# Optimization experiments

Hardware: AMD Instinct MI355X
Metric: run time of the kernel (lower is better)

## Reference

```python
import jax, jax.numpy as jnp
import numpy as np

N_NODES = 100000


def gcn_conv(x, edge_index, W, b):
    """PyG GCNConv: h = x W^T; add self-loops; symmetric deg^-1/2 norm; scatter-add; + bias."""
    n = x.shape[0]
    src = jnp.concatenate([edge_index[0], jnp.arange(n)])  # self-loops appended
    dst = jnp.concatenate([edge_index[1], jnp.arange(n)])
    deg = jax.ops.segment_sum(jnp.ones_like(dst, dtype=x.dtype), dst, num_segments=n)
    dinv = jnp.where(deg > 0, jax.lax.rsqrt(deg), 0.0)
    norm = dinv[src] * dinv[dst]                             # [E+n]
    h = x @ W.T                                              # [n, out]
    msg = norm[:, None] * h[src]                             # [E+n, out] gather
    out = jax.ops.segment_sum(msg, dst, num_segments=n)      # scatter-add
    return out + b


def setup_inputs() -> dict:
    key = jax.random.key(0)
    ks = jax.random.split(key, 10)
    input_dim, gnn_hidden, tree_hidden, num_classes = 128, 64, 32, 8
    n_edges = 3200000
    x = jax.random.normal(ks[0], (N_NODES, input_dim), dtype=jnp.float32)
    edge_index = jax.random.randint(ks[1], (2, n_edges), 0, N_NODES, dtype=jnp.int64)
    # GCNConv params (PyG Linear weight is [out, in], glorot-ish scale)
    W1 = jax.random.normal(ks[2], (gnn_hidden, input_dim), dtype=jnp.float32) / np.sqrt(input_dim)
    b1 = jnp.zeros((gnn_hidden,), dtype=jnp.float32)
    W2 = jax.random.normal(ks[3], (tree_hidden, gnn_hidden), dtype=jnp.float32) / np.sqrt(gnn_hidden)
    b2 = jnp.zeros((tree_hidden,), dtype=jnp.float32)
    # SoftDecisionTree params (torch.randn init in source)
    gate_w = jax.random.normal(ks[4], (tree_hidden, tree_hidden), dtype=jnp.float32)
    gate_b = jnp.zeros((tree_hidden,), dtype=jnp.float32)
    leaf_w = jax.random.normal(ks[5], (tree_hidden, num_classes), dtype=jnp.float32)
    return {"x": x, "edge_index": edge_index, "W1": W1, "b1": b1, "W2": W2,
            "b2": b2, "gate_w": gate_w, "gate_b": gate_b, "leaf_w": leaf_w}


def reference(x, edge_index, W1, b1, W2, b2, gate_w, gate_b, leaf_w):
    h = jax.nn.relu(gcn_conv(x, edge_index, W1, b1))
    h = gcn_conv(h, edge_index, W2, b2)
    gates = jax.nn.sigmoid(h @ gate_w.T + gate_b)
    return gates @ leaf_w
```

## Files before the change

kernel.cpp:

```cpp
#include <hip/hip_runtime.h>
#include <math.h>

#define IN_DIM 128
#define H1 64
#define H2 32
#define NC 8
#define SCAN_CH 1024
#define NB_MAX 512
#define BLK 512
#define CAP 12288

typedef unsigned int u32;

__device__ __forceinline__ float bf_lo(u32 u) { return __uint_as_float(u << 16); }
__device__ __forceinline__ float bf_hi(u32 u) { return __uint_as_float(u & 0xffff0000u); }
__device__ __forceinline__ unsigned short f2b(float f) {
  u32 u = __float_as_uint(f);
  u += 0x7fffu + ((u >> 16) & 1u);
  return (unsigned short)(u >> 16);
}


__global__ __launch_bounds__(256) void k_hist(const int* __restrict__ dst,
                                              int* __restrict__ bh,
                                              int E, int EPB, int NBk) {
  __shared__ int h[NB_MAX];
  int k = blockIdx.x, tid = threadIdx.x;
  for (int i = tid; i < NBk; i += 256) h[i] = 0;
  __syncthreads();
  int st = k * EPB, en = min(E, st + EPB);
  for (int i = st + tid; i < en; i += 256)
    atomicAdd(&h[((u32)dst[i]) >> 8], 1);
  __syncthreads();
  for (int b = tid; b < NBk; b += 256) bh[b * BLK + k] = h[b];
}


__global__ __launch_bounds__(256) void k_gsc1(const int* __restrict__ A,
                                              int* __restrict__ bsum, int L) {
  int b = blockIdx.x, tid = threadIdx.x;
  int i0 = b * SCAN_CH + tid * 4;
  int s = 0;
  if (i0 + 3 < L) {
    int4 v = *(const int4*)(A + i0);
    s = v.x + v.y + v.z + v.w;
  } else {
    for (int i = i0; i < L; ++i) s += A[i];
  }
  __shared__ int red[256];
  red[tid] = s;
  __syncthreads();
  for (int d = 128; d > 0; d >>= 1) {
    if (tid < d) red[tid] += red[tid + d];
    __syncthreads();
  }
  if (tid == 0) bsum[b] = red[0];
}

__global__ __launch_bounds__(256) void k_gsc2(const int* __restrict__ bsum,
                                              int* __restrict__ bbase,
                                              int* __restrict__ S, int nbk, int L) {
  __shared__ int part[256];
  int tid = threadIdx.x;
  int chunk = (nbk + 255) / 256;
  int st = tid * chunk, en = min(st + chunk, nbk);
  int s = 0;
  for (int i = st; i < en; ++i) s += bsum[i];
  part[tid] = s;
  __syncthreads();
  for (int d = 1; d < 256; d <<= 1) {
    int t = (tid >= d) ? part[tid - d] : 0;
    __syncthreads();
    part[tid] += t;
    __syncthreads();
  }
  int base = (tid == 0) ? 0 : part[tid - 1];
  for (int i = st; i < en; ++i) { bbase[i] = base; base += bsum[i]; }
  if (tid == 255) S[L] = part[255];
}

__global__ __launch_bounds__(256) void k_gsc3(const int* __restrict__ A,
                                              const int* __restrict__ bbase,
                                              int* __restrict__ S, int L) {
  int b = blockIdx.x, tid = threadIdx.x;
  int i0 = b * SCAN_CH + tid * 4;
  int e0 = 0, e1 = 0, e2 = 0, e3 = 0;
  if (i0 + 3 < L) {
    int4 v = *(const int4*)(A + i0);
    e0 = v.x; e1 = v.y; e2 = v.z; e3 = v.w;
  } else {
    if (i0 + 0 < L) e0 = A[i0 + 0];
    if (i0 + 1 < L) e1 = A[i0 + 1];
    if (i0 + 2 < L) e2 = A[i0 + 2];
    if (i0 + 3 < L) e3 = A[i0 + 3];
  }
  __shared__ int part[256];
  part[tid] = e0 + e1 + e2 + e3;
  __syncthreads();
  for (int d = 1; d < 256; d <<= 1) {
    int t = (tid >= d) ? part[tid - d] : 0;
    __syncthreads();
    part[tid] += t;
    __syncthreads();
  }
  int base = bbase[b] + ((tid == 0) ? 0 : part[tid - 1]);
  int o0 = base, o1 = o0 + e0, o2 = o1 + e1, o3 = o2 + e2;
  if (i0 + 3 < L) {
    int4 o; o.x = o0; o.y = o1; o.z = o2; o.w = o3;
    *(int4*)(S + i0) = o;
  } else {
    if (i0 + 0 < L) S[i0 + 0] = o0;
    if (i0 + 1 < L) S[i0 + 1] = o1;
    if (i0 + 2 < L) S[i0 + 2] = o2;
    if (i0 + 3 < L) S[i0 + 3] = o3;
  }
}


__global__ __launch_bounds__(256) void k_scatter(const int* __restrict__ src,
                                                 const int* __restrict__ dst,
                                                 const int* __restrict__ S,
                                                 u32* __restrict__ packed,
                                                 int E, int EPB, int NBk) {
  __shared__ int cur[NB_MAX];
  int k = blockIdx.x, tid = threadIdx.x;
  for (int b = tid; b < NBk; b += 256) cur[b] = S[b * BLK + k];
  __syncthreads();
  int st = k * EPB, en = min(E, st + EPB);
  for (int i = st + tid; i < en; i += 256) {
    int d = dst[i];
    int b = ((u32)d) >> 8;
    int pos = atomicAdd(&cur[b], 1);
    packed[pos] = (((u32)d & 255u) << 17) | (u32)src[i];
  }
}


__global__ __launch_bounds__(256) void k_build(const u32* __restrict__ packed,
                                               const int* __restrict__ S,
                                               int* __restrict__ csr,
                                               int* __restrict__ off,
                                               float* __restrict__ dinv,
                                               int n, int NBk) {
  __shared__ int cnt[256];
  __shared__ int tmp[256];
  __shared__ int cur[256];
  __shared__ int sbuf[CAP];
  int b = blockIdx.x, tid = threadIdx.x;
  int r0 = S[b * BLK];
  int r1 = S[(b + 1) * BLK];
  int m = r1 - r0;
  cnt[tid] = 0;
  __syncthreads();
  for (int i = r0 + tid; i < r1; i += 256)
    atomicAdd(&cnt[packed[i] >> 17], 1);
  __syncthreads();
  int v = cnt[tid];
  tmp[tid] = v;
  __syncthreads();
  for (int d = 1; d < 256; d <<= 1) {
    int t = (tid >= d) ? tmp[tid - d] : 0;
    __syncthreads();
    tmp[tid] += t;
    __syncthreads();
  }
  int rel = tmp[tid] - v;
  int node = b * 256 + tid;
  if (node < n) {
    off[node] = r0 + rel;
    dinv[node] = rsqrtf((float)(v + 1));
  }
  if (b == NBk - 1 && tid == 0) off[n] = r1;
  cur[tid] = rel;
  __syncthreads();
  if (m <= CAP) {
    for (int i = r0 + tid; i < r1; i += 256) {
      u32 u = packed[i];
      int pos = atomicAdd(&cur[u >> 17], 1);
      sbuf[pos] = (int)(u & 0x1FFFFu);
    }
    __syncthreads();
    for (int j = tid; j < m; j += 256)
      csr[r0 + j] = sbuf[j];
  } else {
    for (int i = r0 + tid; i < r1; i += 256) {
      u32 u = packed[i];
      int pos = atomicAdd(&cur[u >> 17], 1);
      csr[r0 + pos] = (int)(u & 0x1FFFFu);
    }
  }
}


__global__ void k_proj1(const float4* __restrict__ x4, const float* __restrict__ W1,
                        const float* __restrict__ dinv,
                        unsigned short* __restrict__ h1p, int n) {
  __shared__ float xs[16][IN_DIM];
  __shared__ float wt[IN_DIM][H1 + 1];
  int tid = threadIdx.x;
  int row0 = blockIdx.x * 16;

  for (int i = tid; i < (H1 * IN_DIM / 4); i += 256) {
    float4 w = ((const float4*)W1)[i];
    int o = (i * 4) / IN_DIM;
    int k = (i * 4) % IN_DIM;
    wt[k + 0][o] = w.x; wt[k + 1][o] = w.y; wt[k + 2][o] = w.z; wt[k + 3][o] = w.w;
  }
  for (int i = tid; i < 16 * IN_DIM / 4; i += 256) {
    int r = (i * 4) / IN_DIM, k = (i * 4) % IN_DIM;
    int row = row0 + r;
    if (row < n)
      *((float4*)&xs[r][k]) = x4[(size_t)row * (IN_DIM / 4) + k / 4];
  }
  __syncthreads();

  int o = tid & 63, rq = tid >> 6;
  float a0 = 0.f, a1 = 0.f, a2 = 0.f, a3 = 0.f;
  for (int k = 0; k < IN_DIM; ++k) {
    float w = wt[k][o];
    a0 += xs[rq * 4 + 0][k] * w;
    a1 += xs[rq * 4 + 1][k] * w;
    a2 += xs[rq * 4 + 2][k] * w;
    a3 += xs[rq * 4 + 3][k] * w;
  }
  int r = row0 + rq * 4;
  if (r + 0 < n) h1p[(size_t)(r + 0) * H1 + o] = f2b(a0 * dinv[r + 0]);
  if (r + 1 < n) h1p[(size_t)(r + 1) * H1 + o] = f2b(a1 * dinv[r + 1]);
  if (r + 2 < n) h1p[(size_t)(r + 2) * H1 + o] = f2b(a2 * dinv[r + 2]);
  if (r + 3 < n) h1p[(size_t)(r + 3) * H1 + o] = f2b(a3 * dinv[r + 3]);
}


#define ACC8(v) do { \
    a0 += bf_lo((v).x); a1 += bf_hi((v).x); \
    a2 += bf_lo((v).y); a3 += bf_hi((v).y); \
    a4 += bf_lo((v).z); a5 += bf_hi((v).z); \
    a6 += bf_lo((v).w); a7 += bf_hi((v).w); } while (0)

#define RED8(m) do { \
    a0 += __shfl_xor(a0, m, 64); a1 += __shfl_xor(a1, m, 64); \
    a2 += __shfl_xor(a2, m, 64); a3 += __shfl_xor(a3, m, 64); \
    a4 += __shfl_xor(a4, m, 64); a5 += __shfl_xor(a5, m, 64); \
    a6 += __shfl_xor(a6, m, 64); a7 += __shfl_xor(a7, m, 64); } while (0)

__global__ __launch_bounds__(256) void k_agg64_proj2(
    const u32* __restrict__ hp,
    const float* __restrict__ dinv,
    const int* __restrict__ off, const int* __restrict__ csr,
    const float* __restrict__ b1, const float* __restrict__ W2,
    unsigned short* __restrict__ h2p, int n) {
  __shared__ float wt[H1][H2 + 1];
  __shared__ float rows[4][2][H1];
  __shared__ float b1s[H1];
  int tid = threadIdx.x;

  for (int i = tid; i < H2 * H1 / 4; i += 256) {
    float4 w = ((const float4*)W2)[i];
    int o = (i * 4) / H1, k = (i * 4) % H1;
    wt[k + 0][o] = w.x; wt[k + 1][o] = w.y; wt[k + 2][o] = w.z; wt[k + 3][o] = w.w;
  }
  if (tid < 16) ((float4*)b1s)[tid] = ((const float4*)b1)[tid];
  __syncthreads();

  int lane = tid & 63;
  int wv = __builtin_amdgcn_readfirstlane(tid >> 6);
  int p0n = (blockIdx.x * 4 + wv) * 2;
  int p0c = min(p0n, n - 1);
  int p1c = min(p0n + 1, n - 1);
  int g = lane >> 3, j = lane & 7;
  int nh = g >> 2;

  int tt = 0;
  if (lane < 3) tt = off[min(p0n + lane, n)];
  int r00 = __shfl(tt, 0, 64);
  int r01 = __shfl(tt, 1, 64);
  int r11 = __shfl(tt, 2, 64);
  float dv = 0.f;
  if (lane < 2) dv = dinv[min(p0n + lane, n - 1)];
  float d0 = __shfl(dv, 0, 64), d1 = __shfl(dv, 1, 64);

  const uint4* __restrict__ hp4 = (const uint4*)hp;
  float a0 = 0.f, a1 = 0.f, a2 = 0.f, a3 = 0.f,
        a4 = 0.f, a5 = 0.f, a6 = 0.f, a7 = 0.f;

  if ((g & 3) == 0) {
    uint4 v = hp4[(size_t)(nh ? p1c : p0c) * (H1 / 8) + j];
    ACC8(v);
  }

  int mx = max(r01 - r00, r11 - r01);
  for (int kk = 0; kk * 16 < mx; ++kk) {
    int b0 = r00 + 16 * kk, b1e = r01 + 16 * kk;
    int ci = (lane < 32) ? min(b0 + (lane & 15), r01 - 1)
                         : min(b1e + (lane & 15), r11 - 1);
    int s = csr[max(ci, 0)];
#pragma unroll
    for (int it = 0; it < 4; ++it) {
      int e = it * 4 + (g & 3);
      int sv = __shfl(s, (nh ? 32 : 0) + e, 64);
      int eidx = (nh ? b1e : b0) + e;
      int lim = nh ? r11 : r01;
      if (eidx < lim) {
        uint4 v = hp4[(size_t)sv * (H1 / 8) + j];
        ACC8(v);
      }
    }
  }
  RED8(8); RED8(16);

  float d = (lane < 32) ? d0 : d1;
  if ((lane & 31) < 8) {
    int jj = lane & 7, nn = lane >> 5;
    float4 v0, v1;
    v0.x = fmaxf(a0 * d + b1s[8 * jj + 0], 0.f);
    v0.y = fmaxf(a1 * d + b1s[8 * jj + 1], 0.f);
    v0.z = fmaxf(a2 * d + b1s[8 * jj + 2], 0.f);
    v0.w = fmaxf(a3 * d + b1s[8 * jj + 3], 0.f);
    v1.x = fmaxf(a4 * d + b1s[8 * jj + 4], 0.f);
    v1.y = fmaxf(a5 * d + b1s[8 * jj + 5], 0.f);
    v1.z = fmaxf(a6 * d + b1s[8 * jj + 6], 0.f);
    v1.w = fmaxf(a7 * d + b1s[8 * jj + 7], 0.f);
    *(float4*)&rows[wv][nn][8 * jj + 0] = v0;
    *(float4*)&rows[wv][nn][8 * jj + 4] = v1;
  }
  __syncthreads();

  int node = lane >> 5, o = lane & 31;
  float a = 0.f;
#pragma unroll
  for (int k = 0; k < H1; ++k) a += rows[wv][node][k] * wt[k][o];
  int wout = p0n + node;
  if (wout < n) h2p[(size_t)wout * H2 + o] = f2b(a * ((node) ? d1 : d0));
}


__global__ __launch_bounds__(256) void k_agg32_tree(
    const u32* __restrict__ hp,
    const float* __restrict__ dinv,
    const int* __restrict__ off, const int* __restrict__ csr,
    const float* __restrict__ b2, const float* __restrict__ gate_w,
    const float* __restrict__ gate_b, const float* __restrict__ leaf_w,
    float* __restrict__ out, int n) {
  __shared__ float gwt[H2][H2 + 1];
  __shared__ float lws[H2][NC + 1];
  __shared__ float rowh[4][2][H2];
  __shared__ float rowg[4][2][H2];
  __shared__ float b2s[H2];
  int tid = threadIdx.x;

  {
    float4 w = ((const float4*)gate_w)[tid];
    int jj = (tid * 4) / H2, k = (tid * 4) % H2;
    gwt[k + 0][jj] = w.x; gwt[k + 1][jj] = w.y; gwt[k + 2][jj] = w.z; gwt[k + 3][jj] = w.w;
  }
  lws[tid >> 3][tid & 7] = leaf_w[tid];
  if (tid < 8) ((float4*)b2s)[tid] = ((const float4*)b2)[tid];
  __syncthreads();

  int lane = tid & 63;
  int wv = __builtin_amdgcn_readfirstlane(tid >> 6);
  int p0n = (blockIdx.x * 4 + wv) * 2;
  int p0c = min(p0n, n - 1);
  int p1c = min(p0n + 1, n - 1);
  int g = lane >> 2, j = lane & 3;
  int nh = g >> 3;

  int tt = 0;
  if (lane < 3) tt = off[min(p0n + lane, n)];
  int r00 = __shfl(tt, 0, 64);
  int r01 = __shfl(tt, 1, 64);
  int r11 = __shfl(tt, 2, 64);
  float dv = 0.f;
  if (lane < 2) dv = dinv[min(p0n + lane, n - 1)];
  float d0 = __shfl(dv, 0, 64), d1 = __shfl(dv, 1, 64);

  const uint4* __restrict__ hp4 = (const uint4*)hp;
  float a0 = 0.f, a1 = 0.f, a2 = 0.f, a3 = 0.f,
        a4 = 0.f, a5 = 0.f, a6 = 0.f, a7 = 0.f;

  if ((g & 7) == 0) {
    uint4 v = hp4[(size_t)(nh ? p1c : p0c) * (H2 / 8) + j];
    ACC8(v);
  }

  int mx = max(r01 - r00, r11 - r01);
  for (int kk = 0; kk * 16 < mx; ++kk) {
    int b0 = r00 + 16 * kk, b1e = r01 + 16 * kk;
    int ci = (lane < 32) ? min(b0 + (lane & 15), r01 - 1)
                         : min(b1e + (lane & 15), r11 - 1);
    int s = csr[max(ci, 0)];
#pragma unroll
    for (int it = 0; it < 2; ++it) {
      int e = it * 8 + (g & 7);
      int sv = __shfl(s, (nh ? 32 : 0) + e, 64);
      int eidx = (nh ? b1e : b0) + e;
      int lim = nh ? r11 : r01;
      if (eidx < lim) {
        uint4 v = hp4[(size_t)sv * (H2 / 8) + j];
        ACC8(v);
      }
    }
  }
  RED8(4); RED8(8); RED8(16);

  float d = (lane < 32) ? d0 : d1;
  if ((lane & 31) < 4) {
    int jj = lane & 3, nn = lane >> 5;
    float4 v0, v1;
    v0.x = a0 * d + b2s[8 * jj + 0];
    v0.y = a1 * d + b2s[8 * jj + 1];
    v0.z = a2 * d + b2s[8 * jj + 2];
    v0.w = a3 * d + b2s[8 * jj + 3];
    v1.x = a4 * d + b2s[8 * jj + 4];
    v1.y = a5 * d + b2s[8 * jj + 5];
    v1.z = a6 * d + b2s[8 * jj + 6];
    v1.w = a7 * d + b2s[8 * jj + 7];
    *(float4*)&rowh[wv][nn][8 * jj + 0] = v0;
    *(float4*)&rowh[wv][nn][8 * jj + 4] = v1;
  }
  __syncthreads();

  int node = lane >> 5, f = lane & 31;
  float gacc = 0.f;
#pragma unroll
  for (int k = 0; k < H2; ++k) gacc += rowh[wv][node][k] * gwt[k][f];
  rowg[wv][node][f] = 1.0f / (1.0f + __expf(-(gacc + gate_b[f])));
  __syncthreads();

  int c = lane & 7, gi = (lane >> 3) & 3;
  float a = 0.f;
#pragma unroll
  for (int j8 = 0; j8 < 8; ++j8) {
    int jj = gi * 8 + j8;
    a += rowg[wv][node][jj] * lws[jj][c];
  }
  a += __shfl_xor(a, 8, 64);
  a += __shfl_xor(a, 16, 64);
  int wout = p0n + node;
  if ((lane & 31) < 8 && wout < n) out[(size_t)wout * NC + c] = a;
}


static inline size_t align256(size_t x) { return (x + 255) & ~(size_t)255; }

extern "C" void kernel_launch(void* const* d_in, const int* in_sizes, int n_in,
                              void* d_out, int out_size, void* d_ws, size_t ws_size,
                              hipStream_t stream) {
  const float* x  = (const float*)d_in[0];
  const int*   ei = (const int*)d_in[1];
  const float* W1 = (const float*)d_in[2];
  const float* b1 = (const float*)d_in[3];
  const float* W2 = (const float*)d_in[4];
  const float* b2 = (const float*)d_in[5];
  const float* gw = (const float*)d_in[6];
  const float* gb = (const float*)d_in[7];
  const float* lw = (const float*)d_in[8];
  float* out = (float*)d_out;

  int n = in_sizes[0] / IN_DIM;
  int E = in_sizes[1] / 2;
  const int* src  = ei;
  const int* dstp = ei + E;

  int NBk = (n + 255) >> 8;
  int EPB = (E + BLK - 1) / BLK;
  int L   = NBk * BLK;
  int nbs = (L + SCAN_CH - 1) / SCAN_CH;

  char* w = (char*)d_ws;
  unsigned short* h1p = (unsigned short*)w;  w += align256((size_t)n * H1 * 2);
  unsigned short* h2p = (unsigned short*)w;  w += align256((size_t)n * H2 * 2);
  int* csr    = (int*)w;   w += align256((size_t)E * 4);
  u32* packed = (u32*)w;   w += align256((size_t)E * 4);
  int* bh     = (int*)w;   w += align256(((size_t)L + 1) * 4);
  int* S      = (int*)w;   w += align256(((size_t)L + 1) * 4);
  int* bsum   = (int*)w;   w += align256((size_t)nbs * 4);
  int* bbase  = (int*)w;   w += align256((size_t)nbs * 4);
  float* dinv = (float*)w; w += align256((size_t)n * 4);
  int* off    = (int*)w;   w += align256(((size_t)n + 1) * 4);

  int gw8 = (n + 7) / 8;

  k_hist<<<BLK, 256, 0, stream>>>(dstp, bh, E, EPB, NBk);
  k_gsc1<<<nbs, 256, 0, stream>>>(bh, bsum, L);
  k_gsc2<<<1, 256, 0, stream>>>(bsum, bbase, S, nbs, L);
  k_gsc3<<<nbs, 256, 0, stream>>>(bh, bbase, S, L);
  k_scatter<<<BLK, 256, 0, stream>>>(src, dstp, S, packed, E, EPB, NBk);
  k_build<<<NBk, 256, 0, stream>>>(packed, S, csr, off, dinv, n, NBk);

  k_proj1<<<(n + 15) / 16, 256, 0, stream>>>((const float4*)x, W1, dinv, h1p, n);
  k_agg64_proj2<<<gw8, 256, 0, stream>>>((const u32*)h1p, dinv, off, csr, b1, W2, h2p, n);
  k_agg32_tree<<<gw8, 256, 0, stream>>>((const u32*)h2p, dinv, off, csr, b2, gw, gb, lw, out, n);
}
```

Before: 350.9 us.

## Fuse CSR build stages: single-block scan, global degree, scatter+proj1 merge, sorted neighbors

The histogram kernel now also counts per-node degree with global atomics, which lets dinv be computed early. The three-pass scan collapses into one kernel whose block 0 scans the histogram while the other blocks compute dinv. The edge scatter and the first projection are merged into a single launch with block-range dispatch so they can run concurrently. The build step now sorts each node's neighbors coarsely by source range, which should improve gather locality in the aggregation kernels. The costs are extra global atomics on deg, a single-block scan, larger shared arrays in the build kernel, and the CAP reduction to 10240 that pushes more buckets onto the slower fallback path.

```diff
diff --git a/kernel.cpp b/kernel.cpp
--- a/kernel.cpp
+++ b/kernel.cpp
@@ -5,10 +5,9 @@
 #define H1 64
 #define H2 32
 #define NC 8
-#define SCAN_CH 1024
 #define NB_MAX 512
 #define BLK 512
-#define CAP 12288
+#define CAP 10240
 
 typedef unsigned int u32;
 
@@ -21,185 +20,95 @@
 }
 
 
-__global__ __launch_bounds__(256) void k_hist(const int* __restrict__ dst,
-                                              int* __restrict__ bh,
-                                              int E, int EPB, int NBk) {
+__global__ __launch_bounds__(256) void k_hist2(const int* __restrict__ dst,
+                                               int* __restrict__ bh,
+                                               int* __restrict__ deg,
+                                               int E, int EPB, int NBk) {
   __shared__ int h[NB_MAX];
   int k = blockIdx.x, tid = threadIdx.x;
   for (int i = tid; i < NBk; i += 256) h[i] = 0;
   __syncthreads();
   int st = k * EPB, en = min(E, st + EPB);
-  for (int i = st + tid; i < en; i += 256)
-    atomicAdd(&h[((u32)dst[i]) >> 8], 1);
-  __syncthreads();
-  for (int b = tid; b < NBk; b += 256) bh[b * BLK + k] = h[b];
-}
-
-
-__global__ __launch_bounds__(256) void k_gsc1(const int* __restrict__ A,
-                                              int* __restrict__ bsum, int L) {
-  int b = blockIdx.x, tid = threadIdx.x;
-  int i0 = b * SCAN_CH + tid * 4;
-  int s = 0;
-  if (i0 + 3 < L) {
-    int4 v = *(const int4*)(A + i0);
-    s = v.x + v.y + v.z + v.w;
-  } else {
-    for (int i = i0; i < L; ++i) s += A[i];
-  }
-  __shared__ int red[256];
-  red[tid] = s;
-  __syncthreads();
-  for (int d = 128; d > 0; d >>= 1) {
-    if (tid < d) red[tid] += red[tid + d];
-    __syncthreads();
-  }
-  if (tid == 0) bsum[b] = red[0];
-}
-
-__global__ __launch_bounds__(256) void k_gsc2(const int* __restrict__ bsum,
-                                              int* __restrict__ bbase,
-                                              int* __restrict__ S, int nbk, int L) {
-  __shared__ int part[256];
-  int tid = threadIdx.x;
-  int chunk = (nbk + 255) / 256;
-  int st = tid * chunk, en = min(st + chunk, nbk);
-  int s = 0;
-  for (int i = st; i < en; ++i) s += bsum[i];
-  part[tid] = s;
-  __syncthreads();
-  for (int d = 1; d < 256; d <<= 1) {
-    int t = (tid >= d) ? part[tid - d] : 0;
-    __syncthreads();
-    part[tid] += t;
-    __syncthreads();
-  }
-  int base = (tid == 0) ? 0 : part[tid - 1];
-  for (int i = st; i < en; ++i) { bbase[i] = base; base += bsum[i]; }
-  if (tid == 255) S[L] = part[255];
-}
-
-__global__ __launch_bounds__(256) void k_gsc3(const int* __restrict__ A,
-                                              const int* __restrict__ bbase,
-                                              int* __restrict__ S, int L) {
-  int b = blockIdx.x, tid = threadIdx.x;
-  int i0 = b * SCAN_CH + tid * 4;
-  int e0 = 0, e1 = 0, e2 = 0, e3 = 0;
-  if (i0 + 3 < L) {
-    int4 v = *(const int4*)(A + i0);
-    e0 = v.x; e1 = v.y; e2 = v.z; e3 = v.w;
-  } else {
-    if (i0 + 0 < L) e0 = A[i0 + 0];
-    if (i0 + 1 < L) e1 = A[i0 + 1];
-    if (i0 + 2 < L) e2 = A[i0 + 2];
-    if (i0 + 3 < L) e3 = A[i0 + 3];
-  }
-  __shared__ int part[256];
-  part[tid] = e0 + e1 + e2 + e3;
-  __syncthreads();
-  for (int d = 1; d < 256; d <<= 1) {
-    int t = (tid >= d) ? part[tid - d] : 0;
-    __syncthreads();
-    part[tid] += t;
-    __syncthreads();
-  }
-  int base = bbase[b] + ((tid == 0) ? 0 : part[tid - 1]);
-  int o0 = base, o1 = o0 + e0, o2 = o1 + e1, o3 = o2 + e2;
-  if (i0 + 3 < L) {
-    int4 o; o.x = o0; o.y = o1; o.z = o2; o.w = o3;
-    *(int4*)(S + i0) = o;
-  } else {
-    if (i0 + 0 < L) S[i0 + 0] = o0;
-    if (i0 + 1 < L) S[i0 + 1] = o1;
-    if (i0 + 2 < L) S[i0 + 2] = o2;
-    if (i0 + 3 < L) S[i0 + 3] = o3;
-  }
-}
-
-
-__global__ __launch_bounds__(256) void k_scatter(const int* __restrict__ src,
-                                                 const int* __restrict__ dst,
-                                                 const int* __restrict__ S,
-                                                 u32* __restrict__ packed,
-                                                 int E, int EPB, int NBk) {
-  __shared__ int cur[NB_MAX];
-  int k = blockIdx.x, tid = threadIdx.x;
-  for (int b = tid; b < NBk; b += 256) cur[b] = S[b * BLK + k];
-  __syncthreads();
-  int st = k * EPB, en = min(E, st + EPB);
   for (int i = st + tid; i < en; i += 256) {
     int d = dst[i];
-    int b = ((u32)d) >> 8;
-    int pos = atomicAdd(&cur[b], 1);
-    packed[pos] = (((u32)d & 255u) << 17) | (u32)src[i];
-  }
-}
-
-
-__global__ __launch_bounds__(256) void k_build(const u32* __restrict__ packed,
-                                               const int* __restrict__ S,
-                                               int* __restrict__ csr,
-                                               int* __restrict__ off,
-                                               float* __restrict__ dinv,
-                                               int n, int NBk) {
-  __shared__ int cnt[256];
-  __shared__ int tmp[256];
-  __shared__ int cur[256];
-  __shared__ int sbuf[CAP];
-  int b = blockIdx.x, tid = threadIdx.x;
-  int r0 = S[b * BLK];
-  int r1 = S[(b + 1) * BLK];
-  int m = r1 - r0;
-  cnt[tid] = 0;
-  __syncthreads();
-  for (int i = r0 + tid; i < r1; i += 256)
-    atomicAdd(&cnt[packed[i] >> 17], 1);
-  __syncthreads();
-  int v = cnt[tid];
-  tmp[tid] = v;
-  __syncthreads();
-  for (int d = 1; d < 256; d <<= 1) {
-    int t = (tid >= d) ? tmp[tid - d] : 0;
+    atomicAdd(&h[((u32)d) >> 8], 1);
+    atomicAdd(&deg[d], 1);
+  }
+  __syncthreads();
+  for (int b = tid; b < NBk; b += 256) bh[b * BLK + k] = h[b];
+}
+
+
+__global__ __launch_bounds__(1024) void k_scan_dinv(const int* __restrict__ A,
+                                                    int* __restrict__ S,
+                                                    const int* __restrict__ deg,
+                                                    float* __restrict__ dinv,
+                                                    int L, int n) {
+  if (blockIdx.x == 0) {
+    __shared__ int part[1024];
+    int t = threadIdx.x;
+    int C = (L + 1023) >> 10;
+    C = (C + 3) & ~3;
+    int st = t * C, en = min(st + C, L);
+    int s = 0;
+    int i = st;
+    for (; i + 3 < en; i += 4) {
+      int4 v = *(const int4*)(A + i);
+      s += v.x + v.y + v.z + v.w;
+    }
+    for (; i < en; ++i) s += A[i];
+    part[t] = s;
     __syncthreads();
-    tmp[tid] += t;
-    __syncthreads();
-  }
-  int rel = tmp[tid] - v;
-  int node = b * 256 + tid;
-  if (node < n) {
-    off[node] = r0 + rel;
-    dinv[node] = rsqrtf((float)(v + 1));
-  }
-  if (b == NBk - 1 && tid == 0) off[n] = r1;
-  cur[tid] = rel;
-  __syncthreads();
-  if (m <= CAP) {
-    for (int i = r0 + tid; i < r1; i += 256) {
-      u32 u = packed[i];
-      int pos = atomicAdd(&cur[u >> 17], 1);
-      sbuf[pos] = (int)(u & 0x1FFFFu);
-    }
-    __syncthreads();
-    for (int j = tid; j < m; j += 256)
-      csr[r0 + j] = sbuf[j];
+    for (int d = 1; d < 1024; d <<= 1) {
+      int v = (t >= d) ? part[t - d] : 0;
+      __syncthreads();
+      part[t] += v;
+      __syncthreads();
+    }
+    int base = (t == 0) ? 0 : part[t - 1];
+    i = st;
+    for (; i + 3 < en; i += 4) {
+      int4 v = *(const int4*)(A + i);
+      int4 o;
+      o.x = base; o.y = base + v.x; o.z = o.y + v.y; o.w = o.z + v.z;
+      *(int4*)(S + i) = o;
+      base = o.w + v.w;
+    }
+    for (; i < en; ++i) { S[i] = base; base += A[i]; }
+    if (t == 1023) S[L] = part[1023];
   } else {
-    for (int i = r0 + tid; i < r1; i += 256) {
-      u32 u = packed[i];
-      int pos = atomicAdd(&cur[u >> 17], 1);
-      csr[r0 + pos] = (int)(u & 0x1FFFFu);
-    }
-  }
-}
-
-
-__global__ void k_proj1(const float4* __restrict__ x4, const float* __restrict__ W1,
-                        const float* __restrict__ dinv,
-                        unsigned short* __restrict__ h1p, int n) {
+    int i = (blockIdx.x - 1) * 1024 + threadIdx.x;
+    if (i < n) dinv[i] = rsqrtf((float)(deg[i] + 1));
+  }
+}
+
+
+__global__ __launch_bounds__(256) void k_scat_proj(
+    const int* __restrict__ src, const int* __restrict__ dst,
+    const int* __restrict__ S, u32* __restrict__ packed,
+    int E, int EPB, int NBk,
+    const float4* __restrict__ x4, const float* __restrict__ W1,
+    const float* __restrict__ dinv, unsigned short* __restrict__ h1p, int n) {
+  __shared__ int cur[NB_MAX];
   __shared__ float xs[16][IN_DIM];
   __shared__ float wt[IN_DIM][H1 + 1];
   int tid = threadIdx.x;
-  int row0 = blockIdx.x * 16;
-
+
+  if ((int)blockIdx.x < BLK) {
+    int k = blockIdx.x;
+    for (int b = tid; b < NBk; b += 256) cur[b] = S[b * BLK + k];
+    __syncthreads();
+    int st = k * EPB, en = min(E, st + EPB);
+    for (int i = st + tid; i < en; i += 256) {
+      int d = dst[i];
+      int b = ((u32)d) >> 8;
+      int pos = atomicAdd(&cur[b], 1);
+      packed[pos] = (((u32)d & 255u) << 17) | (u32)src[i];
+    }
+    return;
+  }
+
+  int row0 = ((int)blockIdx.x - BLK) * 16;
   for (int i = tid; i < (H1 * IN_DIM / 4); i += 256) {
     float4 w = ((const float4*)W1)[i];
     int o = (i * 4) / IN_DIM;
@@ -228,6 +137,70 @@
   if (r + 1 < n) h1p[(size_t)(r + 1) * H1 + o] = f2b(a1 * dinv[r + 1]);
   if (r + 2 < n) h1p[(size_t)(r + 2) * H1 + o] = f2b(a2 * dinv[r + 2]);
   if (r + 3 < n) h1p[(size_t)(r + 3) * H1 + o] = f2b(a3 * dinv[r + 3]);
+}
+
+
+__global__ __launch_bounds__(256) void k_build3(const u32* __restrict__ packed,
+                                                const int* __restrict__ S,
+                                                u32* __restrict__ csr2,
+                                                int* __restrict__ off,
+                                                int n, int NBk) {
+  __shared__ int bins[2048];
+  __shared__ int cur[2048];
+  __shared__ int scn[256];
+  __shared__ u32 sbuf[CAP];
+  int b = blockIdx.x, tid = threadIdx.x;
+  int r0 = S[b * BLK];
+  int r1 = S[(b + 1) * BLK];
+  int m = r1 - r0;
+  for (int i = tid; i < 2048; i += 256) bins[i] = 0;
+  __syncthreads();
+  for (int i = r0 + tid; i < r1; i += 256) {
+    u32 p = packed[i];
+    int key = (int)((p >> 17) << 3) | (int)((p & 0x1FFFFu) >> 14);
+    atomicAdd(&bins[key], 1);
+  }
+  __syncthreads();
+  int s = 0;
+#pragma unroll
+  for (int u = 0; u < 8; ++u) s += bins[tid * 8 + u];
+  scn[tid] = s;
+  __syncthreads();
+  for (int d = 1; d < 256; d <<= 1) {
+    int t = (tid >= d) ? scn[tid - d] : 0;
+    __syncthreads();
+    scn[tid] += t;
+    __syncthreads();
+  }
+  int base = scn[tid] - s;
+  int node = b * 256 + tid;
+  if (node < n) off[node] = r0 + base;
+  if (b == NBk - 1 && tid == 0) off[n] = r1;
+#pragma unroll
+  for (int u = 0; u < 8; ++u) {
+    int k = tid * 8 + u;
+    cur[k] = base;
+    base += bins[k];
+  }
+  __syncthreads();
+  if (m <= CAP) {
+    for (int i = r0 + tid; i < r1; i += 256) {
+      u32 p = packed[i];
+      int key = (int)((p >> 17) << 3) | (int)((p & 0x1FFFFu) >> 14);
+      int pos = atomicAdd(&cur[key], 1);
+      sbuf[pos] = p & 0x1FFFFu;
+    }
+    __syncthreads();
+    for (int j = tid; j < m; j += 256)
+      csr2[r0 + j] = sbuf[j];
+  } else {
+    for (int i = r0 + tid; i < r1; i += 256) {
+      u32 p = packed[i];
+      int key = (int)((p >> 17) << 3) | (int)((p & 0x1FFFFu) >> 14);
+      int pos = atomicAdd(&cur[key], 1);
+      csr2[r0 + pos] = p & 0x1FFFFu;
+    }
+  }
 }
 
 
@@ -465,30 +438,29 @@
   int NBk = (n + 255) >> 8;
   int EPB = (E + BLK - 1) / BLK;
   int L   = NBk * BLK;
-  int nbs = (L + SCAN_CH - 1) / SCAN_CH;
 
   char* w = (char*)d_ws;
   unsigned short* h1p = (unsigned short*)w;  w += align256((size_t)n * H1 * 2);
   unsigned short* h2p = (unsigned short*)w;  w += align256((size_t)n * H2 * 2);
-  int* csr    = (int*)w;   w += align256((size_t)E * 4);
+  u32* csr2   = (u32*)w;   w += align256((size_t)E * 4);
   u32* packed = (u32*)w;   w += align256((size_t)E * 4);
   int* bh     = (int*)w;   w += align256(((size_t)L + 1) * 4);
   int* S      = (int*)w;   w += align256(((size_t)L + 1) * 4);
-  int* bsum   = (int*)w;   w += align256((size_t)nbs * 4);
-  int* bbase  = (int*)w;   w += align256((size_t)nbs * 4);
+  int* deg    = (int*)w;   w += align256((size_t)n * 4);
   float* dinv = (float*)w; w += align256((size_t)n * 4);
   int* off    = (int*)w;   w += align256(((size_t)n + 1) * 4);
 
   int gw8 = (n + 7) / 8;
-
-  k_hist<<<BLK, 256, 0, stream>>>(dstp, bh, E, EPB, NBk);
-  k_gsc1<<<nbs, 256, 0, stream>>>(bh, bsum, L);
-  k_gsc2<<<1, 256, 0, stream>>>(bsum, bbase, S, nbs, L);
-  k_gsc3<<<nbs, 256, 0, stream>>>(bh, bbase, S, L);
-  k_scatter<<<BLK, 256, 0, stream>>>(src, dstp, S, packed, E, EPB, NBk);
-  k_build<<<NBk, 256, 0, stream>>>(packed, S, csr, off, dinv, n, NBk);
-
-  k_proj1<<<(n + 15) / 16, 256, 0, stream>>>((const float4*)x, W1, dinv, h1p, n);
-  k_agg64_proj2<<<gw8, 256, 0, stream>>>((const u32*)h1p, dinv, off, csr, b1, W2, h2p, n);
-  k_agg32_tree<<<gw8, 256, 0, stream>>>((const u32*)h2p, dinv, off, csr, b2, gw, gb, lw, out, n);
-}
+  int pblk = (n + 15) / 16;
+
+  hipMemsetAsync(deg, 0, (size_t)n * 4, stream);
+  k_hist2<<<BLK, 256, 0, stream>>>(dstp, bh, deg, E, EPB, NBk);
+  k_scan_dinv<<<1 + (n + 1023) / 1024, 1024, 0, stream>>>(bh, S, deg, dinv, L, n);
+  k_scat_proj<<<BLK + pblk, 256, 0, stream>>>(src, dstp, S, packed, E, EPB, NBk,
+                                              (const float4*)x, W1, dinv, h1p, n);
+  k_build3<<<NBk, 256, 0, stream>>>(packed, S, csr2, off, n, NBk);
+  k_agg64_proj2<<<gw8, 256, 0, stream>>>((const u32*)h1p, dinv, off, (const int*)csr2,
+                                         b1, W2, h2p, n);
+  k_agg32_tree<<<gw8, 256, 0, stream>>>((const u32*)h2p, dinv, off, (const int*)csr2,
+                                        b2, gw, gb, lw, out, n);
+}
```

Measured after the change: 558.0 us. 1.59x slower.

## Sort CSR neighbors by coarse source bucket and vectorize proj1 shared reads

Applied to the files above, without the earlier changes.

The CSR build now bins edges by destination node plus the top bits of the source index (8 sub-buckets per node), so each node's neighbor list is roughly sorted by source region. This is meant to improve gather locality in the two aggregation kernels. The shared staging buffer is shrunk to make room for the larger bin arrays, so more buckets may fall back to direct global scatter. The proj1 inner loop is also changed to read rows of x with float4 from shared memory and unroll four k-steps.

```diff
diff --git a/kernel.cpp b/kernel.cpp
--- a/kernel.cpp
+++ b/kernel.cpp
@@ -8,7 +8,7 @@
 #define SCAN_CH 1024
 #define NB_MAX 512
 #define BLK 512
-#define CAP 12288
+#define CAP 10240
 
 typedef unsigned int u32;
 
@@ -136,57 +136,69 @@
 }
 
 
-__global__ __launch_bounds__(256) void k_build(const u32* __restrict__ packed,
-                                               const int* __restrict__ S,
-                                               int* __restrict__ csr,
-                                               int* __restrict__ off,
-                                               float* __restrict__ dinv,
-                                               int n, int NBk) {
-  __shared__ int cnt[256];
-  __shared__ int tmp[256];
-  __shared__ int cur[256];
-  __shared__ int sbuf[CAP];
+__global__ __launch_bounds__(256) void k_build3(const u32* __restrict__ packed,
+                                                const int* __restrict__ S,
+                                                u32* __restrict__ csr2,
+                                                int* __restrict__ off,
+                                                float* __restrict__ dinv,
+                                                int n, int NBk) {
+  __shared__ int bins[2048];
+  __shared__ int cur[2048];
+  __shared__ int scn[256];
+  __shared__ u32 sbuf[CAP];
   int b = blockIdx.x, tid = threadIdx.x;
   int r0 = S[b * BLK];
   int r1 = S[(b + 1) * BLK];
   int m = r1 - r0;
-  cnt[tid] = 0;
-  __syncthreads();
-  for (int i = r0 + tid; i < r1; i += 256)
-    atomicAdd(&cnt[packed[i] >> 17], 1);
-  __syncthreads();
-  int v = cnt[tid];
-  tmp[tid] = v;
+  for (int i = tid; i < 2048; i += 256) bins[i] = 0;
+  __syncthreads();
+  for (int i = r0 + tid; i < r1; i += 256) {
+    u32 p = packed[i];
+    int key = (int)((p >> 17) << 3) | (int)((p & 0x1FFFFu) >> 14);
+    atomicAdd(&bins[key], 1);
+  }
+  __syncthreads();
+  int s = 0;
+#pragma unroll
+  for (int u = 0; u < 8; ++u) s += bins[tid * 8 + u];
+  scn[tid] = s;
   __syncthreads();
   for (int d = 1; d < 256; d <<= 1) {
-    int t = (tid >= d) ? tmp[tid - d] : 0;
-    __syncthreads();
-    tmp[tid] += t;
-    __syncthreads();
-  }
-  int rel = tmp[tid] - v;
+    int t = (tid >= d) ? scn[tid - d] : 0;
+    __syncthreads();
+    scn[tid] += t;
+    __syncthreads();
+  }
+  int base = scn[tid] - s;
   int node = b * 256 + tid;
   if (node < n) {
-    off[node] = r0 + rel;
-    dinv[node] = rsqrtf((float)(v + 1));
+    off[node] = r0 + base;
+    dinv[node] = rsqrtf((float)(s + 1));
   }
   if (b == NBk - 1 && tid == 0) off[n] = r1;
-  cur[tid] = rel;
+#pragma unroll
+  for (int u = 0; u < 8; ++u) {
+    int k = tid * 8 + u;
+    cur[k] = base;
+    base += bins[k];
+  }
   __syncthreads();
   if (m <= CAP) {
     for (int i = r0 + tid; i < r1; i += 256) {
-      u32 u = packed[i];
-      int pos = atomicAdd(&cur[u >> 17], 1);
-      sbuf[pos] = (int)(u & 0x1FFFFu);
+      u32 p = packed[i];
+      int key = (int)((p >> 17) << 3) | (int)((p & 0x1FFFFu) >> 14);
+      int pos = atomicAdd(&cur[key], 1);
+      sbuf[pos] = p & 0x1FFFFu;
     }
     __syncthreads();
     for (int j = tid; j < m; j += 256)
-      csr[r0 + j] = sbuf[j];
+      csr2[r0 + j] = sbuf[j];
   } else {
     for (int i = r0 + tid; i < r1; i += 256) {
-      u32 u = packed[i];
-      int pos = atomicAdd(&cur[u >> 17], 1);
-      csr[r0 + pos] = (int)(u & 0x1FFFFu);
+      u32 p = packed[i];
+      int key = (int)((p >> 17) << 3) | (int)((p & 0x1FFFFu) >> 14);
+      int pos = atomicAdd(&cur[key], 1);
+      csr2[r0 + pos] = p & 0x1FFFFu;
     }
   }
 }
@@ -215,13 +227,20 @@
   __syncthreads();
 
   int o = tid & 63, rq = tid >> 6;
+  const float4* xr0 = (const float4*)&xs[rq * 4 + 0][0];
+  const float4* xr1 = (const float4*)&xs[rq * 4 + 1][0];
+  const float4* xr2 = (const float4*)&xs[rq * 4 + 2][0];
+  const float4* xr3 = (const float4*)&xs[rq * 4 + 3][0];
   float a0 = 0.f, a1 = 0.f, a2 = 0.f, a3 = 0.f;
-  for (int k = 0; k < IN_DIM; ++k) {
-    float w = wt[k][o];
-    a0 += xs[rq * 4 + 0][k] * w;
-    a1 += xs[rq * 4 + 1][k] * w;
-    a2 += xs[rq * 4 + 2][k] * w;
-    a3 += xs[rq * 4 + 3][k] * w;
+#pragma unroll 4
+  for (int k4 = 0; k4 < IN_DIM / 4; ++k4) {
+    float w0 = wt[4 * k4 + 0][o], w1 = wt[4 * k4 + 1][o],
+          w2 = wt[4 * k4 + 2][o], w3 = wt[4 * k4 + 3][o];
+    float4 v0 = xr0[k4], v1 = xr1[k4], v2 = xr2[k4], v3 = xr3[k4];
+    a0 += v0.x * w0 + v0.y * w1 + v0.z * w2 + v0.w * w3;
+    a1 += v1.x * w0 + v1.y * w1 + v1.z * w2 + v1.w * w3;
+    a2 += v2.x * w0 + v2.y * w1 + v2.z * w2 + v2.w * w3;
+    a3 += v3.x * w0 + v3.y * w1 + v3.z * w2 + v3.w * w3;
   }
   int r = row0 + rq * 4;
   if (r + 0 < n) h1p[(size_t)(r + 0) * H1 + o] = f2b(a0 * dinv[r + 0]);
@@ -470,7 +489,7 @@
   char* w = (char*)d_ws;
   unsigned short* h1p = (unsigned short*)w;  w += align256((size_t)n * H1 * 2);
   unsigned short* h2p = (unsigned short*)w;  w += align256((size_t)n * H2 * 2);
-  int* csr    = (int*)w;   w += align256((size_t)E * 4);
+  u32* csr2   = (u32*)w;   w += align256((size_t)E * 4);
   u32* packed = (u32*)w;   w += align256((size_t)E * 4);
   int* bh     = (int*)w;   w += align256(((size_t)L + 1) * 4);
   int* S      = (int*)w;   w += align256(((size_t)L + 1) * 4);
@@ -486,9 +505,10 @@
   k_gsc2<<<1, 256, 0, stream>>>(bsum, bbase, S, nbs, L);
   k_gsc3<<<nbs, 256, 0, stream>>>(bh, bbase, S, L);
   k_scatter<<<BLK, 256, 0, stream>>>(src, dstp, S, packed, E, EPB, NBk);
-  k_build<<<NBk, 256, 0, stream>>>(packed, S, csr, off, dinv, n, NBk);
-
+  k_build3<<<NBk, 256, 0, stream>>>(packed, S, csr2, off, dinv, n, NBk);
   k_proj1<<<(n + 15) / 16, 256, 0, stream>>>((const float4*)x, W1, dinv, h1p, n);
-  k_agg64_proj2<<<gw8, 256, 0, stream>>>((const u32*)h1p, dinv, off, csr, b1, W2, h2p, n);
-  k_agg32_tree<<<gw8, 256, 0, stream>>>((const u32*)h2p, dinv, off, csr, b2, gw, gb, lw, out, n);
-}
+  k_agg64_proj2<<<gw8, 256, 0, stream>>>((const u32*)h1p, dinv, off, (const int*)csr2,
+                                         b1, W2, h2p, n);
+  k_agg32_tree<<<gw8, 256, 0, stream>>>((const u32*)h2p, dinv, off, (const int*)csr2,
+                                        b2, gw, gb, lw, out, n);
+}
```

Result: slower. 359.5 us (+2.5%).
